# Optimization experiments

Measured on AMD Instinct MI355X. Metric: run time of the kernel, lower is better.

Reference implementation:

```python
import jax, jax.numpy as jnp
import numpy as np

GAMMA = 0.25
GN_EPS = 1e-5


def setup_inputs() -> dict:
    key = jax.random.key(0)
    k1, k2, k3 = jax.random.split(key, 3)
    B, T, C = 16, 2048, 512
    G, V, Dv = 2, 320, 256
    x = jax.random.normal(k1, (B, T, C), dtype=jnp.float32)
    conv_w = jax.random.normal(k2, (G, C // G, C // G), dtype=jnp.float32) * 0.05
    gn_w = jnp.ones((C,), dtype=jnp.float32)
    gn_b = jnp.zeros((C,), dtype=jnp.float32)
    emb = 0.01 * jax.random.normal(k3, (V, G, Dv), dtype=jnp.float32)
    return {"x": x, "conv_w": conv_w, "gn_w": gn_w, "gn_b": gn_b, "emb": emb}


def _vq_forward(x, conv_w, gn_w, gn_b, emb):
    B, T, C = x.shape
    V, G, Dv = emb.shape
    sg = jax.lax.stop_gradient
    # time_first -> BxCxT
    xt = jnp.transpose(x, (0, 2, 1))  # [B,C,T]
    # grouped 1x1 conv (no bias)
    xg = xt.reshape(B, G, C // G, T)
    ze = jnp.einsum('goi,bgit->bgot', conv_w, xg)  # [B,G,C/G,T]
    # Fp32GroupNorm over (C/G, T) per group, biased variance
    zf = ze.astype(jnp.float32)
    mu = jnp.mean(zf, axis=(2, 3), keepdims=True)
    var = jnp.mean(jnp.square(zf - mu), axis=(2, 3), keepdims=True)
    zn = ((zf - mu) * jax.lax.rsqrt(var + GN_EPS)).reshape(B, C, T)
    ze = (zn * gn_w[None, :, None] + gn_b[None, :, None]).astype(ze.dtype)  # [B,C,T]
    # split into groups along feature dim: [B,T,G,Dv]
    ze_ = jnp.transpose(ze.reshape(B, G, Dv, T), (0, 3, 1, 2))
    # squared distances [V,B,T,G] (argmin of ||.||_2 == argmin of ||.||_2^2)
    d2 = (jnp.sum(jnp.square(ze_), axis=-1)[None]
          - 2.0 * jnp.einsum('btgd,vgd->vbtg', ze_, emb)
          + jnp.sum(jnp.square(emb), axis=-1)[:, None, None, :])
    idx = jnp.argmin(d2, axis=0)  # [B,T,G] int
    # gather nearest codewords per group
    zq = emb[idx, jnp.arange(G)[None, None, :]]  # [B,T,G,Dv]
    zq = jnp.transpose(zq.reshape(B, T, C), (0, 2, 1))  # [B,C,T]
    # straight-through
    out = sg(zq) + (ze - sg(ze))  # [B,C,T]
    # code perplexity (no grad)
    probs = jnp.mean(jax.nn.one_hot(sg(idx), V, dtype=jnp.float32), axis=(0, 1))  # [G,V]
    perplexity = jnp.sum(jnp.exp(-jnp.sum(probs * jnp.log(probs + 1e-7), axis=-1)))
    # losses
    zef, zqf = ze.astype(jnp.float32), zq.astype(jnp.float32)
    latent = jnp.mean(jnp.square(zqf - sg(zef)))
    commit = jnp.mean(jnp.square(zef - sg(zqf)))
    loss = latent + GAMMA * commit
    out = jnp.transpose(out, (0, 2, 1))  # back to BxTxC
    return out, loss, perplexity, idx


def reference(x, conv_w, gn_w, gn_b, emb):
    return _vq_forward(x, conv_w, gn_w, gn_b, emb)
```

## Files before the change

### kernel.cpp

```cpp
#include <hip/hip_runtime.h>

#define Bq 16
#define Tq 2048
#define Cq 512
#define Gq 2
#define CGq 256
#define Vq 320
#define Mq 32768
#define LOSS_OFF 16777216
#define PPL_OFF  16777217
#define IDX_OFF  16777218

#define MARGIN 1.75e-4f
#define LIST_CAP 16384
#define LIST2_CAP 1024

#define WS_PCONV 0
#define WS_PLOSS 16384
#define WS_MU    49152
#define WS_RS    49280
#define WS_E2    49408
#define WS_LOSSF 51968
#define WS_CNT   51976
#define WS_CNT2  51980
#define WS_HIST  51984
#define WS_PL2   54544
#define WS_LIST2 70928
#define WS_WSP   131072
#define WS_LISTQ 917504
#define WS_ESP   1048576

#define SL(X, r) ((X) * 16 + ((r) ^ ((X) & 7)))

typedef short s16x8 __attribute__((ext_vector_type(8)));
typedef float f32x4v __attribute__((ext_vector_type(4)));

__device__ __forceinline__ void bsplit(float x, unsigned &b1, unsigned &b2) {
    unsigned u = __float_as_uint(x);
    unsigned r1 = (u + 0x7fffu + ((u >> 16) & 1u)) & 0xffff0000u;
    b1 = r1 >> 16;
    float d = x - __uint_as_float(r1);
    unsigned u2 = __float_as_uint(d);
    b2 = (u2 + 0x7fffu + ((u2 >> 16) & 1u)) >> 16;
}

__device__ __forceinline__ void bsplit3(float x, unsigned &h, unsigned &m, unsigned &l) {
    unsigned u = __float_as_uint(x);
    unsigned r1 = (u + 0x7fffu + ((u >> 16) & 1u)) & 0xffff0000u;
    h = r1 >> 16;
    float d1 = x - __uint_as_float(r1);
    unsigned u2 = __float_as_uint(d1);
    unsigned r2 = (u2 + 0x7fffu + ((u2 >> 16) & 1u)) & 0xffff0000u;
    m = r2 >> 16;
    float d2 = d1 - __uint_as_float(r2);
    unsigned u3 = __float_as_uint(d2);
    l = (u3 + 0x7fffu + ((u3 >> 16) & 1u)) >> 16;
}

__global__ __launch_bounds__(256) void k_prep(const float* __restrict__ w,
                                              const float* __restrict__ emb,
                                              unsigned char* __restrict__ wsp,
                                              unsigned char* __restrict__ esp,
                                              float* __restrict__ e2w) {
    int bx = blockIdx.x, tid = threadIdx.x;
    if (bx < 64) {
        int t = bx * 256 + tid;
        int g = t >> 13, o = (t >> 5) & 255, ihi = t & 31;
        const float* src = w + ((size_t)(g * 256 + o)) * 256 + ihi * 8;
        float xv[8];
        *(float4*)(xv + 0) = *(const float4*)(src);
        *(float4*)(xv + 4) = *(const float4*)(src + 4);
        unsigned ph[4] = {0,0,0,0}, pm[4] = {0,0,0,0}, pl[4] = {0,0,0,0};
#pragma unroll
        for (int e = 0; e < 8; e++) {
            unsigned h, m, l;
            bsplit3(xv[e], h, m, l);
            ph[e >> 1] |= h << ((e & 1) * 16);
            pm[e >> 1] |= m << ((e & 1) * 16);
            pl[e >> 1] |= l << ((e & 1) * 16);
        }
        int kc = ihi >> 2, quad = ihi & 3, ct = o >> 4, lf = o & 15;
        size_t base = (size_t)(g * 3) * 131072 + (size_t)kc * 16384 + ct * 1024 + quad * 256 + lf * 16;
        *(uint4*)(wsp + base + 0 * 131072) = *(uint4*)ph;
        *(uint4*)(wsp + base + 1 * 131072) = *(uint4*)pm;
        *(uint4*)(wsp + base + 2 * 131072) = *(uint4*)pl;
    } else if (bx < 224) {
        int row  = (bx - 64) * 4 + (tid >> 6);
        int lane = tid & 63;
        float4 v = *(const float4*)(emb + (size_t)row * 256 + lane * 4);
        float s = v.x * v.x + v.y * v.y + v.z * v.z + v.w * v.w;
#pragma unroll
        for (int m = 1; m < 64; m <<= 1) s += __shfl_xor(s, m);
        if (lane == 0) e2w[(row & 1) * Vq + (row >> 1)] = s;
    } else {
        int t = (bx - 224) * 256 + tid;
        int g  = t / 10240;
        int r  = t - g * 10240;
        int kc = r / 1280;
        int r2 = r - kc * 1280;
        int ct = r2 >> 6;
        int r3 = r2 & 63;
        int kq = r3 >> 4, l15 = r3 & 15;
        int v  = ct * 16 + l15;
        int k0 = kc * 32 + kq * 8;
        const float* src = emb + ((size_t)v * 2 + g) * 256 + k0;
        float xv[8];
        *(float4*)(xv + 0) = *(const float4*)(src);
        *(float4*)(xv + 4) = *(const float4*)(src + 4);
        unsigned ph[4] = {0,0,0,0}, pl[4] = {0,0,0,0};
#pragma unroll
        for (int e = 0; e < 8; e++) {
            unsigned h, l;
            bsplit(xv[e], h, l);
            ph[e >> 1] |= h << ((e & 1) * 16);
            pl[e >> 1] |= l << ((e & 1) * 16);
        }
        size_t base = (size_t)g * 327680 + (size_t)kc * 20480
                    + (size_t)((ct * 4 + kq) * 16 + l15) * 16;
        *(uint4*)(esp + base) = *(uint4*)ph;
        *(uint4*)(esp + base + 163840) = *(uint4*)pl;
    }
}

__global__ __launch_bounds__(256, 2) void k_convM(const float* __restrict__ x,
    const unsigned char* __restrict__ wsp, float* __restrict__ ze,
    double* __restrict__ pconv)
{
    __shared__ unsigned char lds[73728];
    __shared__ double reds[4], redq[4];
    uint4* Bs = (uint4*)lds;
    uint4* As = (uint4*)(lds + 49152);

    int tid = threadIdx.x, bx = blockIdx.x;
    int mt = bx >> 1, g = bx & 1;
    int m0 = mt * 128;
    int w = tid >> 6, lane = tid & 63;
    int quad = lane >> 4, l15 = lane & 15;
    int arow = tid >> 1, ah = tid & 1;
    int aw = arow >> 5, art = (arow >> 4) & 1, ar = arow & 15;
    const float* xrow = x + (size_t)(m0 + arow) * Cq + g * CGq + ah * 16;
    const unsigned char* wslab = wsp + (size_t)(g * 3) * 131072;

    f32x4v zero4 = {0.f, 0.f, 0.f, 0.f};
    f32x4v acc[2][16];
#pragma unroll
    for (int i = 0; i < 2; i++)
#pragma unroll
        for (int j = 0; j < 16; j++) acc[i][j] = zero4;

    for (int kc = 0; kc < 8; kc++) {
        if (kc) __syncthreads();
#pragma unroll
        for (int j = 0; j < 12; j++) {
            int L = (w * 12 + j) * 1024 + lane * 16;
            int p = L >> 14, r = L & 16383;
            __builtin_amdgcn_global_load_lds(
                (const __attribute__((address_space(1))) void*)(wslab + (size_t)p * 131072 + (size_t)kc * 16384 + r),
                (__attribute__((address_space(3))) void*)(lds + L), 16, 0, 0);
        }
        float xv[16];
        *(float4*)(xv + 0)  = *(const float4*)(xrow + kc * 32 + 0);
        *(float4*)(xv + 4)  = *(const float4*)(xrow + kc * 32 + 4);
        *(float4*)(xv + 8)  = *(const float4*)(xrow + kc * 32 + 8);
        *(float4*)(xv + 12) = *(const float4*)(xrow + kc * 32 + 12);
#pragma unroll
        for (int ii = 0; ii < 2; ii++) {
            unsigned ph[4] = {0,0,0,0}, pm[4] = {0,0,0,0}, pl[4] = {0,0,0,0};
#pragma unroll
            for (int e = 0; e < 8; e++) {
                unsigned h, m, l;
                bsplit3(xv[ii * 8 + e], h, m, l);
                ph[e >> 1] |= h << ((e & 1) * 16);
                pm[e >> 1] |= m << ((e & 1) * 16);
                pl[e >> 1] |= l << ((e & 1) * 16);
            }
            int aq = ah * 2 + ii;
            As[SL(((0 * 4 + aw) * 2 + art) * 4 + aq, ar)] = *(uint4*)ph;
            As[SL(((1 * 4 + aw) * 2 + art) * 4 + aq, ar)] = *(uint4*)pm;
            As[SL(((2 * 4 + aw) * 2 + art) * 4 + aq, ar)] = *(uint4*)pl;
        }
        __syncthreads();
        s16x8 afr[3][2];
#pragma unroll
        for (int p = 0; p < 3; p++)
#pragma unroll
            for (int rt = 0; rt < 2; rt++)
                afr[p][rt] = __builtin_bit_cast(s16x8,
                    As[SL(((p * 4 + w) * 2 + rt) * 4 + quad, l15)]);
#pragma unroll
        for (int ct = 0; ct < 16; ct++) {
            s16x8 b0 = __builtin_bit_cast(s16x8, Bs[0 * 1024 + ct * 64 + quad * 16 + l15]);
            s16x8 b1 = __builtin_bit_cast(s16x8, Bs[1 * 1024 + ct * 64 + quad * 16 + l15]);
            s16x8 b2 = __builtin_bit_cast(s16x8, Bs[2 * 1024 + ct * 64 + quad * 16 + l15]);
#pragma unroll
            for (int rt = 0; rt < 2; rt++) {
                acc[rt][ct] = __builtin_amdgcn_mfma_f32_16x16x32_bf16(afr[0][rt], b0, acc[rt][ct], 0, 0, 0);
                acc[rt][ct] = __builtin_amdgcn_mfma_f32_16x16x32_bf16(afr[1][rt], b0, acc[rt][ct], 0, 0, 0);
                acc[rt][ct] = __builtin_amdgcn_mfma_f32_16x16x32_bf16(afr[2][rt], b0, acc[rt][ct], 0, 0, 0);
                acc[rt][ct] = __builtin_amdgcn_mfma_f32_16x16x32_bf16(afr[0][rt], b1, acc[rt][ct], 0, 0, 0);
                acc[rt][ct] = __builtin_amdgcn_mfma_f32_16x16x32_bf16(afr[1][rt], b1, acc[rt][ct], 0, 0, 0);
                acc[rt][ct] = __builtin_amdgcn_mfma_f32_16x16x32_bf16(afr[0][rt], b2, acc[rt][ct], 0, 0, 0);
            }
        }
    }

    float s = 0.f, q = 0.f;
    float* zb = ze + (size_t)m0 * Cq + g * CGq;
#pragma unroll
    for (int rt = 0; rt < 2; rt++)
#pragma unroll
    for (int ct = 0; ct < 16; ct++)
#pragma unroll
    for (int j = 0; j < 4; j++) {
        float v = acc[rt][ct][j];
        zb[(size_t)(w * 32 + rt * 16 + quad * 4 + j) * Cq + ct * 16 + l15] = v;
        s += v;
        q = __builtin_fmaf(v, v, q);
    }
    double ds = (double)s, dq = (double)q;
#pragma unroll
    for (int m = 1; m < 64; m <<= 1) { ds += __shfl_xor(ds, m); dq += __shfl_xor(dq, m); }
    if (lane == 0) { reds[w] = ds; redq[w] = dq; }
    __syncthreads();
    if (tid == 0) {
        pconv[bx * 2 + 0] = reds[0] + reds[1] + reds[2] + reds[3];
        pconv[bx * 2 + 1] = redq[0] + redq[1] + redq[2] + redq[3];
    }
}

__global__ __launch_bounds__(256) void k_stats(const double* __restrict__ pconv,
                                               float* __restrict__ muw,
                                               float* __restrict__ rsw) {
    int tid = threadIdx.x;
    int bg = tid >> 3, r = tid & 7;
    int b = bg >> 1, g = bg & 1;
    double s = 0.0, q = 0.0;
    for (int j = r; j < 16; j += 8) {
        int pi = (b * 16 + j) * 2 + g;
        s += pconv[pi * 2 + 0];
        q += pconv[pi * 2 + 1];
    }
#pragma unroll
    for (int m = 1; m < 8; m <<= 1) { s += __shfl_xor(s, m); q += __shfl_xor(q, m); }
    if (r == 0) {
        double mu = s / 524288.0;
        double var = q / 524288.0 - mu * mu;
        double rs = 1.0 / sqrt(var + 1e-5);
        muw[bg] = (float)mu;
        rsw[bg] = (float)rs;
    }
}

__global__ __launch_bounds__(256, 2) void k_distA(const unsigned char* __restrict__ esp,
    const float* __restrict__ gw, const float* __restrict__ gb,
    const float* __restrict__ muw, const float* __restrict__ rsw,
    const float* __restrict__ e2w, float* dout,
    unsigned* __restrict__ cntw, unsigned* __restrict__ cnt2w,
    unsigned long long* __restrict__ listq, unsigned* __restrict__ list2,
    unsigned* __restrict__ hist, double* __restrict__ ploss)
{
    __shared__ uint4 Asl[1024];
    __shared__ unsigned char ldsB[40960];
    __shared__ float e2s[Vq];
    __shared__ float z2l[128];
    __shared__ double redp[4];
    uint4* Bsl = (uint4*)ldsB;

    int tid = threadIdx.x, bx = blockIdx.x;
    int mt = bx >> 1, g = bx & 1;
    int m0 = mt * 128;
    int bg = (m0 >> 11) * 2 + g;
    float muf = muw[bg], rsf = rsw[bg];
    int w = tid >> 6, lane = tid & 63;
    int quad = lane >> 4, l15 = lane & 15;

    for (int i = tid; i < Vq; i += 256) e2s[i] = e2w[g * Vq + i];

    int arow = tid >> 1, ah = tid & 1;
    int aw = arow >> 5, art = (arow >> 4) & 1, ar = arow & 15;
    const float* zrow = dout + (size_t)m0 * Cq + g * CGq + (size_t)arow * Cq;
    const unsigned char* eslab = esp + (size_t)g * 327680;

    f32x4v zero4 = {0.f, 0.f, 0.f, 0.f};
    f32x4v acc[2][20];
#pragma unroll
    for (int i = 0; i < 2; i++)
#pragma unroll
        for (int j = 0; j < 20; j++) acc[i][j] = zero4;
    float z2acc = 0.f;

    for (int kc8 = 0; kc8 < 8; kc8++) {
        if (kc8) __syncthreads();
        int k0 = kc8 * 32;
#pragma unroll
        for (int j = 0; j < 10; j++) {
            int L = j * 4096 + tid * 16;
            int s = (j >= 5) ? 1 : 0;
            __builtin_amdgcn_global_load_lds(
                (const __attribute__((address_space(1))) void*)(eslab + (size_t)s * 143360 + (size_t)kc8 * 20480 + L),
                (__attribute__((address_space(3))) void*)(ldsB + L), 16, 0, 0);
        }
#pragma unroll
        for (int i2 = 0; i2 < 2; i2++) {
            uint4 o1, o2;
            unsigned hw[4], lw[4];
#pragma unroll
            for (int ii = 0; ii < 2; ii++) {
                int koff = k0 + ah * 16 + i2 * 8 + ii * 4;
                float4 z  = *(const float4*)(zrow + koff);
                float4 gv = *(const float4*)(gw + g * CGq + koff);
                float4 bvv= *(const float4*)(gb + g * CGq + koff);
                float zn0 = (z.x - muf) * rsf * gv.x + bvv.x;
                float zn1 = (z.y - muf) * rsf * gv.y + bvv.y;
                float zn2 = (z.z - muf) * rsf * gv.z + bvv.z;
                float zn3 = (z.w - muf) * rsf * gv.w + bvv.w;
                z2acc = __builtin_fmaf(zn0, zn0, z2acc);
                z2acc = __builtin_fmaf(zn1, zn1, z2acc);
                z2acc = __builtin_fmaf(zn2, zn2, z2acc);
                z2acc = __builtin_fmaf(zn3, zn3, z2acc);
                unsigned h0,l0,h1,l1,h2,l2,h3,l3;
                bsplit(zn0, h0, l0); bsplit(zn1, h1, l1);
                bsplit(zn2, h2, l2); bsplit(zn3, h3, l3);
                hw[ii*2+0] = h0 | (h1 << 16); hw[ii*2+1] = h2 | (h3 << 16);
                lw[ii*2+0] = l0 | (l1 << 16); lw[ii*2+1] = l2 | (l3 << 16);
            }
            o1.x = hw[0]; o1.y = hw[1]; o1.z = hw[2]; o1.w = hw[3];
            o2.x = lw[0]; o2.y = lw[1]; o2.z = lw[2]; o2.w = lw[3];
            int kq = ah * 2 + i2;
            Asl[SL(((0*4 + aw)*2 + art)*4 + kq, ar)] = o1;
            Asl[SL(((1*4 + aw)*2 + art)*4 + kq, ar)] = o2;
        }
        __syncthreads();
        s16x8 afr[2][2];
#pragma unroll
        for (int s = 0; s < 2; s++)
#pragma unroll
            for (int rt = 0; rt < 2; rt++)
                afr[s][rt] = __builtin_bit_cast(s16x8,
                    Asl[SL(((s*4 + w)*2 + rt)*4 + quad, l15)]);
#pragma unroll
        for (int ct = 0; ct < 20; ct++) {
            s16x8 b0 = __builtin_bit_cast(s16x8, Bsl[((0*20 + ct)*4 + quad)*16 + l15]);
            s16x8 b1 = __builtin_bit_cast(s16x8, Bsl[((1*20 + ct)*4 + quad)*16 + l15]);
#pragma unroll
            for (int rt = 0; rt < 2; rt++) {
                acc[rt][ct] = __builtin_amdgcn_mfma_f32_16x16x32_bf16(afr[0][rt], b0, acc[rt][ct], 0, 0, 0);
                acc[rt][ct] = __builtin_amdgcn_mfma_f32_16x16x32_bf16(afr[0][rt], b1, acc[rt][ct], 0, 0, 0);
                acc[rt][ct] = __builtin_amdgcn_mfma_f32_16x16x32_bf16(afr[1][rt], b0, acc[rt][ct], 0, 0, 0);
            }
        }
    }

    {
        float z2pair = z2acc + __shfl_xor(z2acc, 1);
        if (ah == 0) z2l[arow] = z2pair;
    }
    __syncthreads();

    double lacc = 0.0;
#pragma unroll
    for (int rt = 0; rt < 2; rt++)
#pragma unroll
    for (int j = 0; j < 4; j++) {
        float m1 = 3.402823466e+38f; int i1 = 0;
#pragma unroll
        for (int ct = 0; ct < 20; ct++) {
            float d2a = e2s[ct * 16 + l15] - 2.0f * acc[rt][ct][j];
            if (d2a < m1) { m1 = d2a; i1 = ct * 16 + l15; }
        }
#pragma unroll
        for (int mm = 1; mm < 16; mm <<= 1) {
            float ov = __shfl_xor(m1, mm);
            int   oi = __shfl_xor(i1, mm);
            if (ov < m1 || (ov == m1 && oi < i1)) { m1 = ov; i1 = oi; }
        }
        float thr = m1 + MARGIN;
        unsigned mask = 0;
#pragma unroll
        for (int ct = 0; ct < 20; ct++) {
            float d2a = e2s[ct * 16 + l15] - 2.0f * acc[rt][ct][j];
            if (d2a <= thr) mask |= (1u << ct);
        }
        int cnt = __popc(mask);
#pragma unroll
        for (int mm = 1; mm < 16; mm <<= 1) cnt += __shfl_xor(cnt, mm);
        int mrow = m0 + w * 32 + rt * 16 + quad * 4 + j;
        unsigned q = (unsigned)mrow * 2u + (unsigned)g;
        unsigned flag = 0;
        if (cnt > 1) {
            if ((i1 & 15) == l15) mask &= ~(1u << (i1 >> 4));
            int cl2 = __popc(mask);
            int inc = cl2;
#pragma unroll
            for (int off = 1; off < 16; off <<= 1) {
                int t = __shfl_up(inc, off, 16);
                if (l15 >= off) inc += t;
            }
            int pre = inc - cl2;
            if (cnt <= 5) {
                int pos_ = 0;
                if (l15 == 0) pos_ = (int)atomicAdd(cntw, 1u);
                pos_ = __shfl(pos_, 0, 16);
                if ((unsigned)pos_ < LIST_CAP) {
                    flag = 512u;
                    unsigned long long contrib = 0ull;
                    unsigned mm2 = mask; int k = pre;
                    while (mm2) {
                        int ct2 = __ffs(mm2) - 1; mm2 &= mm2 - 1;
                        contrib |= ((unsigned long long)(unsigned)(ct2 * 16 + l15)) << (20 + 9 * k);
                        k++;
                    }
#pragma unroll
                    for (int mm = 1; mm < 16; mm <<= 1)
                        contrib |= __shfl_xor(contrib, mm);
                    if (l15 == 0)
                        listq[pos_] = (unsigned long long)q
                                    | ((unsigned long long)(unsigned)cnt << 17) | contrib;
                }
            } else {
                if (l15 == 0) {
                    unsigned p2 = atomicAdd(cnt2w, 1u);
                    if (p2 < LIST2_CAP) { list2[p2] = q; flag = 512u; }
                }
            }
        }
        if (l15 == 0) {
            if (flag) {
                dout[IDX_OFF + q] = __uint_as_float((unsigned)i1 | flag);
            } else {
                dout[IDX_OFF + q] = (float)i1;
                atomicAdd(&hist[g * Vq + i1], 1u);
                lacc += (double)z2l[mrow - m0] + (double)m1;
            }
        }
    }
#pragma unroll
    for (int mm = 1; mm < 64; mm <<= 1) lacc += __shfl_xor(lacc, mm);
    if (lane == 0) redp[w] = lacc;
    __syncthreads();
    if (tid == 0) ploss[bx] = redp[0] + redp[1] + redp[2] + redp[3];
}

__global__ __launch_bounds__(256) void k_exF(const float* __restrict__ emb,
    const float* __restrict__ gw, const float* __restrict__ gb,
    const float* __restrict__ muw, const float* __restrict__ rsw,
    const float* __restrict__ e2w, float* dout,
    unsigned* __restrict__ hist, double* __restrict__ ploss2,
    const unsigned long long* __restrict__ listq, const unsigned* __restrict__ cntw,
    double* __restrict__ lossf,
    const unsigned* __restrict__ cnt2w, const unsigned* __restrict__ list2)
{
    int tid = threadIdx.x, lane = tid & 63;
    int gwid = blockIdx.x * 4 + (tid >> 6);
    int cslot = lane >> 2, j = lane & 3;
    unsigned nn = *cntw; if (nn > LIST_CAP) nn = LIST_CAP;
    int n = (int)nn;
    double lacc = 0.0;
    for (int it = gwid; it < n; it += 2048) {
        unsigned long long e = listq[it];
        unsigned q = (unsigned)(e & 0x1FFFFull);
        int cnt = (int)((e >> 17) & 7u);
        int m = (int)(q >> 1), g = (int)(q & 1u);
        int bg = (m >> 11) * 2 + g;
        float muf = muw[bg], rsf = rsw[bg];
        int v = (int)(__float_as_uint(dout[IDX_OFF + q]) & 511u);
        if (cslot >= 1 && cslot < cnt)
            v = (int)((e >> (20 + 9 * (cslot - 1))) & 511ull);
        const float* zb  = dout + (size_t)m * Cq + g * CGq;
        const float* gwb = gw + g * CGq;
        const float* gbb = gb + g * CGq;
        const float* eb  = emb + ((size_t)v * Gq + g) * CGq;
        float z2p = 0.f, dp = 0.f;
        for (int kc = 0; kc < 16; kc++) {
            int k0 = kc * 16 + j * 4;
            float4 z  = *(const float4*)(zb + k0);
            float4 gv = *(const float4*)(gwb + k0);
            float4 bv = *(const float4*)(gbb + k0);
            float4 e4 = *(const float4*)(eb + k0);
            float zn0 = __fadd_rn(__fmul_rn(__fmul_rn(__fsub_rn(z.x, muf), rsf), gv.x), bv.x);
            float zn1 = __fadd_rn(__fmul_rn(__fmul_rn(__fsub_rn(z.y, muf), rsf), gv.y), bv.y);
            float zn2 = __fadd_rn(__fmul_rn(__fmul_rn(__fsub_rn(z.z, muf), rsf), gv.z), bv.z);
            float zn3 = __fadd_rn(__fmul_rn(__fmul_rn(__fsub_rn(z.w, muf), rsf), gv.w), bv.w);
            z2p = __builtin_fmaf(zn0, zn0, z2p);
            z2p = __builtin_fmaf(zn1, zn1, z2p);
            z2p = __builtin_fmaf(zn2, zn2, z2p);
            z2p = __builtin_fmaf(zn3, zn3, z2p);
            dp = __builtin_fmaf(zn0, e4.x, dp);
            dp = __builtin_fmaf(zn1, e4.y, dp);
            dp = __builtin_fmaf(zn2, e4.z, dp);
            dp = __builtin_fmaf(zn3, e4.w, dp);
        }
        z2p += __shfl_xor(z2p, 1); z2p += __shfl_xor(z2p, 2);
        dp  += __shfl_xor(dp, 1);  dp  += __shfl_xor(dp, 2);
        float d2 = __fadd_rn(__fsub_rn(z2p, 2.0f * dp), e2w[g * Vq + v]);
#pragma unroll
        for (int mm = 4; mm < 64; mm <<= 1) {
            float od = __shfl_xor(d2, mm);
            int   ov = __shfl_xor(v, mm);
            if (od < d2 || (od == d2 && ov < v)) { d2 = od; v = ov; }
        }
        if (lane == 0) {
            dout[IDX_OFF + q] = (float)v;
            atomicAdd(&hist[g * Vq + v], 1u);
            lacc += (double)d2;
        }
    }
    if (lane == 0) ploss2[gwid] = lacc;

    unsigned nn2 = *cnt2w; if (nn2 > LIST2_CAP) nn2 = LIST2_CAP;
    int n2 = (int)nn2;
    for (int it = gwid; it < n2; it += 2048) {
        int q = (int)list2[it];
        int m = q >> 1, g = q & 1;
        int bg = (m >> 11) * 2 + g;
        float muf = muw[bg], rsf = rsw[bg];
        const float* zb = dout + (size_t)m * Cq + g * CGq;
        int k0 = lane * 4;
        float4 z  = *(const float4*)(zb + k0);
        float4 gv = *(const float4*)(gw + g * CGq + k0);
        float4 bv = *(const float4*)(gb + g * CGq + k0);
        float zn0 = __fadd_rn(__fmul_rn(__fmul_rn(__fsub_rn(z.x, muf), rsf), gv.x), bv.x);
        float zn1 = __fadd_rn(__fmul_rn(__fmul_rn(__fsub_rn(z.y, muf), rsf), gv.y), bv.y);
        float zn2 = __fadd_rn(__fmul_rn(__fmul_rn(__fsub_rn(z.z, muf), rsf), gv.z), bv.z);
        float zn3 = __fadd_rn(__fmul_rn(__fmul_rn(__fsub_rn(z.w, muf), rsf), gv.w), bv.w);
        float s = 0.f;
        for (int kc = 0; kc < 16; kc++) {
            int src = (lane & 3) + kc * 4;
            float a0 = __shfl(zn0, src), a1 = __shfl(zn1, src);
            float a2 = __shfl(zn2, src), a3 = __shfl(zn3, src);
            s = __builtin_fmaf(a0, a0, s);
            s = __builtin_fmaf(a1, a1, s);
            s = __builtin_fmaf(a2, a2, s);
            s = __builtin_fmaf(a3, a3, s);
        }
        s += __shfl_xor(s, 1); s += __shfl_xor(s, 2);
        float z2 = s;
        float m1 = 3.402823466e+38f; int i1 = 0;
        for (int v = 0; v < Vq; v += 2) {
            const float* e0 = emb + ((size_t)v * Gq + g) * CGq + k0;
            float4 ea = *(const float4*)e0;
            float4 eb4 = *(const float4*)(e0 + Gq * CGq);
            float da = zn0 * ea.x;  da = __builtin_fmaf(zn1, ea.y, da);
            da = __builtin_fmaf(zn2, ea.z, da); da = __builtin_fmaf(zn3, ea.w, da);
            float db = zn0 * eb4.x; db = __builtin_fmaf(zn1, eb4.y, db);
            db = __builtin_fmaf(zn2, eb4.z, db); db = __builtin_fmaf(zn3, eb4.w, db);
#pragma unroll
            for (int mm = 1; mm < 64; mm <<= 1) { da += __shfl_xor(da, mm); db += __shfl_xor(db, mm); }
            float d2a = __fadd_rn(__fsub_rn(z2, 2.0f * da), e2w[g * Vq + v]);
            float d2b = __fadd_rn(__fsub_rn(z2, 2.0f * db), e2w[g * Vq + v + 1]);
            if (d2a < m1) { m1 = d2a; i1 = v; }
            if (d2b < m1) { m1 = d2b; i1 = v + 1; }
        }
        if (lane == 0) {
            dout[IDX_OFF + q] = (float)i1;
            atomicAdd(&hist[g * Vq + i1], 1u);
            atomicAdd(lossf, (double)m1);
        }
    }
}

__global__ __launch_bounds__(256) void k_out(const float* __restrict__ emb, float* dout) {
    size_t u = (size_t)blockIdx.x * 256 + threadIdx.x;
    size_t pos = u * 4;
    int m = (int)(pos >> 9);
    int c = (int)(pos & 511);
    int g = c >> 8, d = c & 255;
    int v = (int)dout[IDX_OFF + (size_t)m * Gq + g];
    float4 o = *(const float4*)(emb + ((size_t)(v * 2 + g)) * 256 + d);
    *(float4*)(dout + pos) = o;
}

__global__ __launch_bounds__(256) void k_final(const double* __restrict__ ploss,
                                               const double* __restrict__ ploss2,
                                               const double* __restrict__ lossf,
                                               const unsigned* __restrict__ hist,
                                               float* dout) {
    __shared__ double redl[4], red0[4], red1[4];
    int tid = threadIdx.x;
    double s = 0.0;
    for (int i = tid; i < 512; i += 256) s += ploss[i];
    for (int i = tid; i < 2048; i += 256) s += ploss2[i];
#pragma unroll
    for (int m = 1; m < 64; m <<= 1) s += __shfl_xor(s, m);
    double e0 = 0.0, e1 = 0.0;
    for (int pid = tid; pid < 640; pid += 256) {
        double p = (double)hist[pid] * (1.0 / 32768.0);
        double t = p * log(p + 1e-7);
        if (pid < 320) e0 += t; else e1 += t;
    }
#pragma unroll
    for (int m = 1; m < 64; m <<= 1) { e0 += __shfl_xor(e0, m); e1 += __shfl_xor(e1, m); }
    int lane = tid & 63, wv_ = tid >> 6;
    if (lane == 0) { redl[wv_] = s; red0[wv_] = e0; red1[wv_] = e1; }
    __syncthreads();
    if (tid == 0) {
        double S  = redl[0] + redl[1] + redl[2] + redl[3] + *lossf;
        double E0 = red0[0] + red0[1] + red0[2] + red0[3];
        double E1 = red1[0] + red1[1] + red1[2] + red1[3];
        dout[LOSS_OFF] = (float)(1.25 * S / 16777216.0);
        dout[PPL_OFF]  = (float)(exp(-E0) + exp(-E1));
    }
}

extern "C" void kernel_launch(void* const* d_in, const int* in_sizes, int n_in,
                              void* d_out, int out_size, void* d_ws, size_t ws_size,
                              hipStream_t stream) {
    const float* x   = (const float*)d_in[0];
    const float* w   = (const float*)d_in[1];
    const float* gw  = (const float*)d_in[2];
    const float* gb  = (const float*)d_in[3];
    const float* emb = (const float*)d_in[4];
    float* dout = (float*)d_out;
    char* ws = (char*)d_ws;
    double* pconv   = (double*)(ws + WS_PCONV);
    double* ploss   = (double*)(ws + WS_PLOSS);
    float* muw      = (float*)(ws + WS_MU);
    float* rsw      = (float*)(ws + WS_RS);
    float* e2w      = (float*)(ws + WS_E2);
    double* lossf   = (double*)(ws + WS_LOSSF);
    unsigned* cntw  = (unsigned*)(ws + WS_CNT);
    unsigned* cnt2w = (unsigned*)(ws + WS_CNT2);
    unsigned* hist  = (unsigned*)(ws + WS_HIST);
    double* ploss2  = (double*)(ws + WS_PL2);
    unsigned* list2 = (unsigned*)(ws + WS_LIST2);
    unsigned char* wsp = (unsigned char*)(ws + WS_WSP);
    unsigned long long* listq = (unsigned long long*)(ws + WS_LISTQ);
    unsigned char* esp = (unsigned char*)(ws + WS_ESP);

    hipMemsetAsync(ws + WS_LOSSF, 0, 2576, stream);
    k_prep<<<304, 256, 0, stream>>>(w, emb, wsp, esp, e2w);
    k_convM<<<512, 256, 0, stream>>>(x, wsp, dout, pconv);
    k_stats<<<1, 256, 0, stream>>>(pconv, muw, rsw);
    k_distA<<<512, 256, 0, stream>>>(esp, gw, gb, muw, rsw, e2w, dout,
                                     cntw, cnt2w, listq, list2, hist, ploss);
    k_exF<<<512, 256, 0, stream>>>(emb, gw, gb, muw, rsw, e2w, dout, hist, ploss2,
                                   listq, cntw, lossf, cnt2w, list2);
    k_out<<<16384, 256, 0, stream>>>(emb, dout);
    k_final<<<1, 256, 0, stream>>>(ploss, ploss2, lossf, hist, dout);
}
```

Measured before the change: 160.7 us.

## Use single-bf16 raw conv output for distance GEMM, fold GroupNorm into codebook terms

The distance GEMM now runs on the un-normalized conv output, written by k_convM as single bf16 in a pre-swizzled layout. The GroupNorm affine is folded algebraically into per-codeword constants (s1, c1) and a per-group scale beta. Codebook operands are built on the fly as bf16(emb*gamma) instead of a split hi/lo precomputed slab, cutting the MFMA count from 3 to 1 per tile pair. The exactness margin grows to absorb the lower precision, which may push more rows into the exact refinement path in k_exF.

```diff
diff --git a/kernel.cpp b/kernel.cpp
--- a/kernel.cpp
+++ b/kernel.cpp
@@ -11,37 +11,35 @@
 #define PPL_OFF  16777217
 #define IDX_OFF  16777218
 
-#define MARGIN 1.75e-4f
+#define MARGIN2 6.0e-3f
 #define LIST_CAP 16384
 #define LIST2_CAP 1024
 
 #define WS_PCONV 0
-#define WS_PLOSS 16384
-#define WS_MU    49152
-#define WS_RS    49280
-#define WS_E2    49408
-#define WS_LOSSF 51968
-#define WS_CNT   51976
-#define WS_CNT2  51980
-#define WS_HIST  51984
-#define WS_PL2   54544
-#define WS_LIST2 70928
-#define WS_WSP   131072
-#define WS_LISTQ 917504
-#define WS_ESP   1048576
+#define WS_MU    8192
+#define WS_RS    8320
+#define WS_E2    8448
+#define WS_S1    11008
+#define WS_C1    13568
+#define WS_LOSSF 16128
+#define WS_CNT   16136
+#define WS_CNT2  16140
+#define WS_HIST  16144
+#define WS_WSP   20480
+#define WS_LISTQ 20480
+#define WS_PLOSS 151552
+#define WS_PL2   155648
+#define WS_LIST2 172032
+#define WS_ZSP   806912
 
 #define SL(X, r) ((X) * 16 + ((r) ^ ((X) & 7)))
 
 typedef short s16x8 __attribute__((ext_vector_type(8)));
 typedef float f32x4v __attribute__((ext_vector_type(4)));
 
-__device__ __forceinline__ void bsplit(float x, unsigned &b1, unsigned &b2) {
+__device__ __forceinline__ unsigned rne16(float x) {
     unsigned u = __float_as_uint(x);
-    unsigned r1 = (u + 0x7fffu + ((u >> 16) & 1u)) & 0xffff0000u;
-    b1 = r1 >> 16;
-    float d = x - __uint_as_float(r1);
-    unsigned u2 = __float_as_uint(d);
-    b2 = (u2 + 0x7fffu + ((u2 >> 16) & 1u)) >> 16;
+    return (u + 0x7fffu + ((u >> 16) & 1u)) >> 16;
 }
 
 __device__ __forceinline__ void bsplit3(float x, unsigned &h, unsigned &m, unsigned &l) {
@@ -59,9 +57,12 @@
 
 __global__ __launch_bounds__(256) void k_prep(const float* __restrict__ w,
                                               const float* __restrict__ emb,
+                                              const float* __restrict__ gw,
+                                              const float* __restrict__ gb,
                                               unsigned char* __restrict__ wsp,
-                                              unsigned char* __restrict__ esp,
-                                              float* __restrict__ e2w) {
+                                              float* __restrict__ e2w,
+                                              float* __restrict__ s1w,
+                                              float* __restrict__ c1w) {
     int bx = blockIdx.x, tid = threadIdx.x;
     if (bx < 64) {
         int t = bx * 256 + tid;
@@ -84,47 +85,34 @@
         *(uint4*)(wsp + base + 0 * 131072) = *(uint4*)ph;
         *(uint4*)(wsp + base + 1 * 131072) = *(uint4*)pm;
         *(uint4*)(wsp + base + 2 * 131072) = *(uint4*)pl;
-    } else if (bx < 224) {
+    } else {
         int row  = (bx - 64) * 4 + (tid >> 6);
         int lane = tid & 63;
+        int g = row & 1;
         float4 v = *(const float4*)(emb + (size_t)row * 256 + lane * 4);
         float s = v.x * v.x + v.y * v.y + v.z * v.z + v.w * v.w;
-#pragma unroll
-        for (int m = 1; m < 64; m <<= 1) s += __shfl_xor(s, m);
-        if (lane == 0) e2w[(row & 1) * Vq + (row >> 1)] = s;
-    } else {
-        int t = (bx - 224) * 256 + tid;
-        int g  = t / 10240;
-        int r  = t - g * 10240;
-        int kc = r / 1280;
-        int r2 = r - kc * 1280;
-        int ct = r2 >> 6;
-        int r3 = r2 & 63;
-        int kq = r3 >> 4, l15 = r3 & 15;
-        int v  = ct * 16 + l15;
-        int k0 = kc * 32 + kq * 8;
-        const float* src = emb + ((size_t)v * 2 + g) * 256 + k0;
-        float xv[8];
-        *(float4*)(xv + 0) = *(const float4*)(src);
-        *(float4*)(xv + 4) = *(const float4*)(src + 4);
-        unsigned ph[4] = {0,0,0,0}, pl[4] = {0,0,0,0};
-#pragma unroll
-        for (int e = 0; e < 8; e++) {
-            unsigned h, l;
-            bsplit(xv[e], h, l);
-            ph[e >> 1] |= h << ((e & 1) * 16);
-            pl[e >> 1] |= l << ((e & 1) * 16);
-        }
-        size_t base = (size_t)g * 327680 + (size_t)kc * 20480
-                    + (size_t)((ct * 4 + kq) * 16 + l15) * 16;
-        *(uint4*)(esp + base) = *(uint4*)ph;
-        *(uint4*)(esp + base + 163840) = *(uint4*)pl;
+        float4 g4 = *(const float4*)(gw + g * CGq + lane * 4);
+        float4 b4 = *(const float4*)(gb + g * CGq + lane * 4);
+        float c1 = g4.x * v.x + g4.y * v.y + g4.z * v.z + g4.w * v.w;
+        float c2 = b4.x * v.x + b4.y * v.y + b4.z * v.z + b4.w * v.w;
+#pragma unroll
+        for (int m = 1; m < 64; m <<= 1) {
+            s  += __shfl_xor(s, m);
+            c1 += __shfl_xor(c1, m);
+            c2 += __shfl_xor(c2, m);
+        }
+        if (lane == 0) {
+            int idx = g * Vq + (row >> 1);
+            e2w[idx] = s;
+            s1w[idx] = s - 2.0f * c2;
+            c1w[idx] = c1;
+        }
     }
 }
 
 __global__ __launch_bounds__(256, 2) void k_convM(const float* __restrict__ x,
     const unsigned char* __restrict__ wsp, float* __restrict__ ze,
-    double* __restrict__ pconv)
+    double* __restrict__ pconv, unsigned char* __restrict__ zsp)
 {
     __shared__ unsigned char lds[73728];
     __shared__ double reds[4], redq[4];
@@ -226,6 +214,28 @@
         pconv[bx * 2 + 0] = reds[0] + reds[1] + reds[2] + reds[3];
         pconv[bx * 2 + 1] = redq[0] + redq[1] + redq[2] + redq[3];
     }
+
+    {
+        unsigned short* t16 = (unsigned short*)lds;
+#pragma unroll
+        for (int rt = 0; rt < 2; rt++)
+#pragma unroll
+        for (int ct = 0; ct < 16; ct++)
+#pragma unroll
+        for (int j = 0; j < 4; j++)
+            t16[w * 8448 + (rt * 16 + quad * 4 + j) * 264 + ct * 16 + l15] =
+                (unsigned short)rne16(acc[rt][ct][j]);
+        __syncthreads();
+        uint4* zt = (uint4*)(zsp + (size_t)bx * 65536);
+        int rr = lane & 15, kq = lane >> 4;
+#pragma unroll
+        for (int kc8 = 0; kc8 < 8; kc8++)
+#pragma unroll
+        for (int rt = 0; rt < 2; rt++) {
+            uint4 vf = *(uint4*)&t16[w * 8448 + (rt * 16 + rr) * 264 + kc8 * 32 + kq * 8];
+            zt[((kc8 * 4 + w) * 2 + rt) * 64 + lane] = vf;
+        }
+    }
 }
 
 __global__ __launch_bounds__(256) void k_stats(const double* __restrict__ pconv,
@@ -251,17 +261,19 @@
     }
 }
 
-__global__ __launch_bounds__(256, 2) void k_distA(const unsigned char* __restrict__ esp,
+__global__ __launch_bounds__(256, 2) void k_distA(const unsigned char* __restrict__ zsp,
+    const float* __restrict__ emb,
     const float* __restrict__ gw, const float* __restrict__ gb,
     const float* __restrict__ muw, const float* __restrict__ rsw,
-    const float* __restrict__ e2w, float* dout,
+    const float* __restrict__ s1w, const float* __restrict__ c1w,
+    float* dout,
     unsigned* __restrict__ cntw, unsigned* __restrict__ cnt2w,
     unsigned long long* __restrict__ listq, unsigned* __restrict__ list2,
     unsigned* __restrict__ hist, double* __restrict__ ploss)
 {
-    __shared__ uint4 Asl[1024];
-    __shared__ unsigned char ldsB[40960];
-    __shared__ float e2s[Vq];
+    __shared__ unsigned char ldsA[8192];
+    __shared__ unsigned char ldsB[20480];
+    __shared__ float s0s[Vq];
     __shared__ float z2l[128];
     __shared__ double redp[4];
     uint4* Bsl = (uint4*)ldsB;
@@ -271,15 +283,18 @@
     int m0 = mt * 128;
     int bg = (m0 >> 11) * 2 + g;
     float muf = muw[bg], rsf = rsw[bg];
+    float beta = 2.0f * rsf;
+    float alpha = beta * muf;
     int w = tid >> 6, lane = tid & 63;
     int quad = lane >> 4, l15 = lane & 15;
 
-    for (int i = tid; i < Vq; i += 256) e2s[i] = e2w[g * Vq + i];
+    for (int i = tid; i < Vq; i += 256)
+        s0s[i] = s1w[g * Vq + i] + alpha * c1w[g * Vq + i];
 
     int arow = tid >> 1, ah = tid & 1;
-    int aw = arow >> 5, art = (arow >> 4) & 1, ar = arow & 15;
     const float* zrow = dout + (size_t)m0 * Cq + g * CGq + (size_t)arow * Cq;
-    const unsigned char* eslab = esp + (size_t)g * 327680;
+    const unsigned char* zt = zsp + (size_t)bx * 65536;
+    int bv = tid >> 3, bk4 = (tid & 7) * 4;
 
     f32x4v zero4 = {0.f, 0.f, 0.f, 0.f};
     f32x4v acc[2][20];
@@ -292,18 +307,28 @@
     for (int kc8 = 0; kc8 < 8; kc8++) {
         if (kc8) __syncthreads();
         int k0 = kc8 * 32;
-#pragma unroll
-        for (int j = 0; j < 10; j++) {
-            int L = j * 4096 + tid * 16;
-            int s = (j >= 5) ? 1 : 0;
+        {
+            int Lw = w * 2048 + lane * 16;
             __builtin_amdgcn_global_load_lds(
-                (const __attribute__((address_space(1))) void*)(eslab + (size_t)s * 143360 + (size_t)kc8 * 20480 + L),
-                (__attribute__((address_space(3))) void*)(ldsB + L), 16, 0, 0);
+                (const __attribute__((address_space(1))) void*)(zt + (size_t)kc8 * 8192 + Lw),
+                (__attribute__((address_space(3))) void*)(ldsA + Lw), 16, 0, 0);
+            __builtin_amdgcn_global_load_lds(
+                (const __attribute__((address_space(1))) void*)(zt + (size_t)kc8 * 8192 + Lw + 1024),
+                (__attribute__((address_space(3))) void*)(ldsA + Lw + 1024), 16, 0, 0);
+        }
+#pragma unroll
+        for (int r = 0; r < 10; r++) {
+            int v = r * 32 + bv;
+            float4 e4 = *(const float4*)(emb + ((size_t)v * Gq + g) * CGq + k0 + bk4);
+            float4 g4 = *(const float4*)(gw + g * CGq + k0 + bk4);
+            unsigned h0 = rne16(e4.x * g4.x), h1 = rne16(e4.y * g4.y);
+            unsigned h2 = rne16(e4.z * g4.z), h3 = rne16(e4.w * g4.w);
+            uint2 hv; hv.x = h0 | (h1 << 16); hv.y = h2 | (h3 << 16);
+            int s0 = ((v >> 4) * 4 + (bk4 >> 3)) * 16 + (v & 15);
+            ((uint2*)&Bsl[s0])[(bk4 >> 2) & 1] = hv;
         }
 #pragma unroll
         for (int i2 = 0; i2 < 2; i2++) {
-            uint4 o1, o2;
-            unsigned hw[4], lw[4];
 #pragma unroll
             for (int ii = 0; ii < 2; ii++) {
                 int koff = k0 + ah * 16 + i2 * 8 + ii * 4;
@@ -318,36 +343,19 @@
                 z2acc = __builtin_fmaf(zn1, zn1, z2acc);
                 z2acc = __builtin_fmaf(zn2, zn2, z2acc);
                 z2acc = __builtin_fmaf(zn3, zn3, z2acc);
-                unsigned h0,l0,h1,l1,h2,l2,h3,l3;
-                bsplit(zn0, h0, l0); bsplit(zn1, h1, l1);
-                bsplit(zn2, h2, l2); bsplit(zn3, h3, l3);
-                hw[ii*2+0] = h0 | (h1 << 16); hw[ii*2+1] = h2 | (h3 << 16);
-                lw[ii*2+0] = l0 | (l1 << 16); lw[ii*2+1] = l2 | (l3 << 16);
             }
-            o1.x = hw[0]; o1.y = hw[1]; o1.z = hw[2]; o1.w = hw[3];
-            o2.x = lw[0]; o2.y = lw[1]; o2.z = lw[2]; o2.w = lw[3];
-            int kq = ah * 2 + i2;
-            Asl[SL(((0*4 + aw)*2 + art)*4 + kq, ar)] = o1;
-            Asl[SL(((1*4 + aw)*2 + art)*4 + kq, ar)] = o2;
         }
         __syncthreads();
-        s16x8 afr[2][2];
-#pragma unroll
-        for (int s = 0; s < 2; s++)
+        s16x8 afr[2];
+#pragma unroll
+        for (int rt = 0; rt < 2; rt++)
+            afr[rt] = *(s16x8*)(ldsA + (((w * 2 + rt) * 4 + quad) * 16 + l15) * 16);
+#pragma unroll
+        for (int ct = 0; ct < 20; ct++) {
+            s16x8 b = *(s16x8*)(ldsB + ((ct * 4 + quad) * 16 + l15) * 16);
 #pragma unroll
             for (int rt = 0; rt < 2; rt++)
-                afr[s][rt] = __builtin_bit_cast(s16x8,
-                    Asl[SL(((s*4 + w)*2 + rt)*4 + quad, l15)]);
-#pragma unroll
-        for (int ct = 0; ct < 20; ct++) {
-            s16x8 b0 = __builtin_bit_cast(s16x8, Bsl[((0*20 + ct)*4 + quad)*16 + l15]);
-            s16x8 b1 = __builtin_bit_cast(s16x8, Bsl[((1*20 + ct)*4 + quad)*16 + l15]);
-#pragma unroll
-            for (int rt = 0; rt < 2; rt++) {
-                acc[rt][ct] = __builtin_amdgcn_mfma_f32_16x16x32_bf16(afr[0][rt], b0, acc[rt][ct], 0, 0, 0);
-                acc[rt][ct] = __builtin_amdgcn_mfma_f32_16x16x32_bf16(afr[0][rt], b1, acc[rt][ct], 0, 0, 0);
-                acc[rt][ct] = __builtin_amdgcn_mfma_f32_16x16x32_bf16(afr[1][rt], b0, acc[rt][ct], 0, 0, 0);
-            }
+                acc[rt][ct] = __builtin_amdgcn_mfma_f32_16x16x32_bf16(afr[rt], b, acc[rt][ct], 0, 0, 0);
         }
     }
 
@@ -365,7 +373,7 @@
         float m1 = 3.402823466e+38f; int i1 = 0;
 #pragma unroll
         for (int ct = 0; ct < 20; ct++) {
-            float d2a = e2s[ct * 16 + l15] - 2.0f * acc[rt][ct][j];
+            float d2a = s0s[ct * 16 + l15] - beta * acc[rt][ct][j];
             if (d2a < m1) { m1 = d2a; i1 = ct * 16 + l15; }
         }
 #pragma unroll
@@ -374,11 +382,11 @@
             int   oi = __shfl_xor(i1, mm);
             if (ov < m1 || (ov == m1 && oi < i1)) { m1 = ov; i1 = oi; }
         }
-        float thr = m1 + MARGIN;
+        float thr = m1 + MARGIN2;
         unsigned mask = 0;
 #pragma unroll
         for (int ct = 0; ct < 20; ct++) {
-            float d2a = e2s[ct * 16 + l15] - 2.0f * acc[rt][ct][j];
+            float d2a = s0s[ct * 16 + l15] - beta * acc[rt][ct][j];
             if (d2a <= thr) mask |= (1u << ct);
         }
         int cnt = __popc(mask);
@@ -613,25 +621,27 @@
     float* dout = (float*)d_out;
     char* ws = (char*)d_ws;
     double* pconv   = (double*)(ws + WS_PCONV);
-    double* ploss   = (double*)(ws + WS_PLOSS);
     float* muw      = (float*)(ws + WS_MU);
     float* rsw      = (float*)(ws + WS_RS);
     float* e2w      = (float*)(ws + WS_E2);
+    float* s1w      = (float*)(ws + WS_S1);
+    float* c1w      = (float*)(ws + WS_C1);
     double* lossf   = (double*)(ws + WS_LOSSF);
     unsigned* cntw  = (unsigned*)(ws + WS_CNT);
     unsigned* cnt2w = (unsigned*)(ws + WS_CNT2);
     unsigned* hist  = (unsigned*)(ws + WS_HIST);
+    unsigned char* wsp = (unsigned char*)(ws + WS_WSP);
+    unsigned long long* listq = (unsigned long long*)(ws + WS_LISTQ);
+    double* ploss   = (double*)(ws + WS_PLOSS);
     double* ploss2  = (double*)(ws + WS_PL2);
     unsigned* list2 = (unsigned*)(ws + WS_LIST2);
-    unsigned char* wsp = (unsigned char*)(ws + WS_WSP);
-    unsigned long long* listq = (unsigned long long*)(ws + WS_LISTQ);
-    unsigned char* esp = (unsigned char*)(ws + WS_ESP);
+    unsigned char* zsp = (unsigned char*)(ws + WS_ZSP);
 
     hipMemsetAsync(ws + WS_LOSSF, 0, 2576, stream);
-    k_prep<<<304, 256, 0, stream>>>(w, emb, wsp, esp, e2w);
-    k_convM<<<512, 256, 0, stream>>>(x, wsp, dout, pconv);
+    k_prep<<<224, 256, 0, stream>>>(w, emb, gw, gb, wsp, e2w, s1w, c1w);
+    k_convM<<<512, 256, 0, stream>>>(x, wsp, dout, pconv, zsp);
     k_stats<<<1, 256, 0, stream>>>(pconv, muw, rsw);
-    k_distA<<<512, 256, 0, stream>>>(esp, gw, gb, muw, rsw, e2w, dout,
+    k_distA<<<512, 256, 0, stream>>>(zsp, emb, gw, gb, muw, rsw, s1w, c1w, dout,
                                      cntw, cnt2w, listq, list2, hist, ploss);
     k_exF<<<512, 256, 0, stream>>>(emb, gw, gb, muw, rsw, e2w, dout, hist, ploss2,
                                    listq, cntw, lossf, cnt2w, list2);
```

New measurement: 203.0 us. +26.3%, slower.

## Use single bf16 distance pass with wider rescoring margin instead of split-bf16

Applied to the files above, without the earlier changes.

Replaces the hi/lo bf16 split (three MFMAs per tile) in the distance kernel with a single bf16 product per tile, halving the codebook bytes loaded and the LDS footprint. The candidate margin for exact rescoring widens from 1.75e-4 to 8e-3 so near-ties are still resolved by the existing fallback path. This cuts MFMA work and memory traffic in the main distance GEMM, but sends more rows to the rescoring lists, which could overflow list capacity or add cost downstream.

```diff
diff --git a/kernel.cpp b/kernel.cpp
--- a/kernel.cpp
+++ b/kernel.cpp
@@ -11,7 +11,7 @@
 #define PPL_OFF  16777217
 #define IDX_OFF  16777218
 
-#define MARGIN 1.75e-4f
+#define MARGIN2 8.0e-3f
 #define LIST_CAP 16384
 #define LIST2_CAP 1024
 
@@ -35,13 +35,9 @@
 typedef short s16x8 __attribute__((ext_vector_type(8)));
 typedef float f32x4v __attribute__((ext_vector_type(4)));
 
-__device__ __forceinline__ void bsplit(float x, unsigned &b1, unsigned &b2) {
+__device__ __forceinline__ unsigned rne16(float x) {
     unsigned u = __float_as_uint(x);
-    unsigned r1 = (u + 0x7fffu + ((u >> 16) & 1u)) & 0xffff0000u;
-    b1 = r1 >> 16;
-    float d = x - __uint_as_float(r1);
-    unsigned u2 = __float_as_uint(d);
-    b2 = (u2 + 0x7fffu + ((u2 >> 16) & 1u)) >> 16;
+    return (u + 0x7fffu + ((u >> 16) & 1u)) >> 16;
 }
 
 __device__ __forceinline__ void bsplit3(float x, unsigned &h, unsigned &m, unsigned &l) {
@@ -107,18 +103,15 @@
         float xv[8];
         *(float4*)(xv + 0) = *(const float4*)(src);
         *(float4*)(xv + 4) = *(const float4*)(src + 4);
-        unsigned ph[4] = {0,0,0,0}, pl[4] = {0,0,0,0};
+        unsigned ph[4] = {0,0,0,0};
 #pragma unroll
         for (int e = 0; e < 8; e++) {
-            unsigned h, l;
-            bsplit(xv[e], h, l);
+            unsigned h = rne16(xv[e]);
             ph[e >> 1] |= h << ((e & 1) * 16);
-            pl[e >> 1] |= l << ((e & 1) * 16);
         }
         size_t base = (size_t)g * 327680 + (size_t)kc * 20480
                     + (size_t)((ct * 4 + kq) * 16 + l15) * 16;
         *(uint4*)(esp + base) = *(uint4*)ph;
-        *(uint4*)(esp + base + 163840) = *(uint4*)pl;
     }
 }
 
@@ -259,8 +252,8 @@
     unsigned long long* __restrict__ listq, unsigned* __restrict__ list2,
     unsigned* __restrict__ hist, double* __restrict__ ploss)
 {
-    __shared__ uint4 Asl[1024];
-    __shared__ unsigned char ldsB[40960];
+    __shared__ uint4 Asl[512];
+    __shared__ unsigned char ldsB[20480];
     __shared__ float e2s[Vq];
     __shared__ float z2l[128];
     __shared__ double redp[4];
@@ -293,17 +286,15 @@
         if (kc8) __syncthreads();
         int k0 = kc8 * 32;
 #pragma unroll
-        for (int j = 0; j < 10; j++) {
+        for (int j = 0; j < 5; j++) {
             int L = j * 4096 + tid * 16;
-            int s = (j >= 5) ? 1 : 0;
             __builtin_amdgcn_global_load_lds(
-                (const __attribute__((address_space(1))) void*)(eslab + (size_t)s * 143360 + (size_t)kc8 * 20480 + L),
+                (const __attribute__((address_space(1))) void*)(eslab + (size_t)kc8 * 20480 + L),
                 (__attribute__((address_space(3))) void*)(ldsB + L), 16, 0, 0);
         }
 #pragma unroll
         for (int i2 = 0; i2 < 2; i2++) {
-            uint4 o1, o2;
-            unsigned hw[4], lw[4];
+            unsigned hw[4];
 #pragma unroll
             for (int ii = 0; ii < 2; ii++) {
                 int koff = k0 + ah * 16 + i2 * 8 + ii * 4;
@@ -318,36 +309,22 @@
                 z2acc = __builtin_fmaf(zn1, zn1, z2acc);
                 z2acc = __builtin_fmaf(zn2, zn2, z2acc);
                 z2acc = __builtin_fmaf(zn3, zn3, z2acc);
-                unsigned h0,l0,h1,l1,h2,l2,h3,l3;
-                bsplit(zn0, h0, l0); bsplit(zn1, h1, l1);
-                bsplit(zn2, h2, l2); bsplit(zn3, h3, l3);
-                hw[ii*2+0] = h0 | (h1 << 16); hw[ii*2+1] = h2 | (h3 << 16);
-                lw[ii*2+0] = l0 | (l1 << 16); lw[ii*2+1] = l2 | (l3 << 16);
+                hw[ii*2+0] = rne16(zn0) | (rne16(zn1) << 16);
+                hw[ii*2+1] = rne16(zn2) | (rne16(zn3) << 16);
             }
+            uint4 o1;
             o1.x = hw[0]; o1.y = hw[1]; o1.z = hw[2]; o1.w = hw[3];
-            o2.x = lw[0]; o2.y = lw[1]; o2.z = lw[2]; o2.w = lw[3];
             int kq = ah * 2 + i2;
-            Asl[SL(((0*4 + aw)*2 + art)*4 + kq, ar)] = o1;
-            Asl[SL(((1*4 + aw)*2 + art)*4 + kq, ar)] = o2;
+            Asl[SL((aw * 2 + art) * 4 + kq, ar)] = o1;
         }
         __syncthreads();
-        s16x8 afr[2][2];
-#pragma unroll
-        for (int s = 0; s < 2; s++)
-#pragma unroll
-            for (int rt = 0; rt < 2; rt++)
-                afr[s][rt] = __builtin_bit_cast(s16x8,
-                    Asl[SL(((s*4 + w)*2 + rt)*4 + quad, l15)]);
+        s16x8 afr0 = __builtin_bit_cast(s16x8, Asl[SL((w * 2 + 0) * 4 + quad, l15)]);
+        s16x8 afr1 = __builtin_bit_cast(s16x8, Asl[SL((w * 2 + 1) * 4 + quad, l15)]);
 #pragma unroll
         for (int ct = 0; ct < 20; ct++) {
-            s16x8 b0 = __builtin_bit_cast(s16x8, Bsl[((0*20 + ct)*4 + quad)*16 + l15]);
-            s16x8 b1 = __builtin_bit_cast(s16x8, Bsl[((1*20 + ct)*4 + quad)*16 + l15]);
-#pragma unroll
-            for (int rt = 0; rt < 2; rt++) {
-                acc[rt][ct] = __builtin_amdgcn_mfma_f32_16x16x32_bf16(afr[0][rt], b0, acc[rt][ct], 0, 0, 0);
-                acc[rt][ct] = __builtin_amdgcn_mfma_f32_16x16x32_bf16(afr[0][rt], b1, acc[rt][ct], 0, 0, 0);
-                acc[rt][ct] = __builtin_amdgcn_mfma_f32_16x16x32_bf16(afr[1][rt], b0, acc[rt][ct], 0, 0, 0);
-            }
+            s16x8 b = __builtin_bit_cast(s16x8, Bsl[(ct * 4 + quad) * 16 + l15]);
+            acc[0][ct] = __builtin_amdgcn_mfma_f32_16x16x32_bf16(afr0, b, acc[0][ct], 0, 0, 0);
+            acc[1][ct] = __builtin_amdgcn_mfma_f32_16x16x32_bf16(afr1, b, acc[1][ct], 0, 0, 0);
         }
     }
 
@@ -374,7 +351,7 @@
             int   oi = __shfl_xor(i1, mm);
             if (ov < m1 || (ov == m1 && oi < i1)) { m1 = ov; i1 = oi; }
         }
-        float thr = m1 + MARGIN;
+        float thr = m1 + MARGIN2;
         unsigned mask = 0;
 #pragma unroll
         for (int ct = 0; ct < 20; ct++) {
```

Result: slower. 191.9 us (+19.4%).
